# Kernel tuning notes

Hardware: AMD Instinct MI355X
Metric: run time of the kernel (lower is better)

The kernel has to match this reference:

```python
import jax, jax.numpy as jnp
import numpy as np

NS, B, T, S, H, V, G = 30, 16, 8, 400, 400, 20000, 3


def setup_inputs() -> dict:
    key = jax.random.key(0)
    ks = jax.random.split(key, 16)
    f = lambda k, shp, s: jax.random.normal(k, shp, jnp.float32) * s
    return dict(
        encoded_hidden=f(ks[0], (B, H), 1.0),
        encoded_outputs=f(ks[1], (B, S, H), 1.0),
        slot_emb=f(ks[2], (NS, H), 0.1),
        emb=f(ks[3], (V, H), 0.1),
        W_ih=f(ks[4], (3 * H, H), 0.05),
        W_hh=f(ks[5], (3 * H, H), 0.05),
        b_ih=jnp.zeros((3 * H,), jnp.float32),
        b_hh=jnp.zeros((3 * H,), jnp.float32),
        W_ratio_w=f(ks[6], (1, 3 * H), 0.05),
        W_ratio_b=jnp.zeros((1,), jnp.float32),
        W_gate_w=f(ks[7], (G, H), 0.05),
        W_gate_b=jnp.zeros((G,), jnp.float32),
        story=jax.random.randint(ks[8], (B, S), 0, V),
        target=jax.random.randint(ks[9], (B, NS, T), 0, V),
        encoded_lens=jax.random.randint(ks[10], (B,), S // 2, S + 1).astype(jnp.int32),
    )


def reference(encoded_hidden, encoded_outputs, slot_emb, emb, W_ih, W_hh, b_ih, b_hh,
              W_ratio_w, W_ratio_b, W_gate_w, W_gate_b, story, target, encoded_lens):
    ns, h = slot_emb.shape
    b, s, _ = encoded_outputs.shape
    t = target.shape[2]
    v = emb.shape[0]
    bs = ns * b  # fused slot*batch decode rows (parallel_decode)

    enc_out = jnp.tile(encoded_outputs, (ns, 1, 1))            # [bs,S,H]
    story_r = jnp.tile(story, (ns, 1))                          # [bs,S]
    lens_r = jnp.tile(encoded_lens, (ns,))                      # [bs]
    mask = jnp.arange(s)[None, :] < lens_r[:, None]             # [bs,S]
    h0 = jnp.tile(encoded_hidden, (ns, 1))                      # [bs,H]
    x0 = jnp.broadcast_to(slot_emb[:, None, :], (ns, b, h)).reshape(bs, h)
    # teacher-forcing inputs, slot-major flatten like target[:, :, wi].T.flatten()
    tf_in = emb[jnp.transpose(target, (2, 1, 0)).reshape(t, bs)]  # [T,bs,H]
    row = jnp.arange(bs)[:, None]
    neg_inf = jnp.float32(-jnp.inf)

    def gru_cell(x, hid):
        gi = x @ W_ih.T + b_ih
        gh = hid @ W_hh.T + b_hh
        ir, iz, inn = jnp.split(gi, 3, axis=-1)
        hr, hz, hn = jnp.split(gh, 3, axis=-1)
        r = jax.nn.sigmoid(ir + hr)
        z = jax.nn.sigmoid(iz + hz)
        n = jnp.tanh(inn + r * hn)
        return (1.0 - z) * n + z * hid

    def step(carry, x_next):
        hid, x = carry
        h_new = gru_cell(x, hid)                                # dec_state == hidden for 1-step GRU
        scores = jnp.einsum('bh,bsh->bs', h_new, enc_out)
        scores = jnp.where(mask, scores, neg_inf)
        prob = jax.nn.softmax(scores, axis=1)
        context = jnp.einsum('bs,bsh->bh', prob, enc_out)
        p_vocab = jax.nn.softmax(h_new @ emb.T, axis=1)         # [bs,V]
        p_gen_vec = jnp.concatenate([h_new, context, x], axis=-1)
        switch = jax.nn.sigmoid(p_gen_vec @ W_ratio_w.T + W_ratio_b)  # [bs,1]
        p_ctx = jnp.zeros((bs, v), p_vocab.dtype).at[row, story_r].add(prob)
        final = (1.0 - switch) * p_ctx + switch * p_vocab
        gate = context @ W_gate_w.T + W_gate_b
        return (h_new, x_next), (final, gate)

    _, (finals, gates) = jax.lax.scan(step, (h0, x0), tf_in)
    all_point = finals.reshape(t, ns, b, v).transpose(1, 2, 0, 3)  # [NS,B,T,V]
    all_gate = gates[0].reshape(ns, b, -1)                          # gates from wi==0
    return all_point, all_gate
```

## Files before the change

kernel.cpp:

```cpp
#include <hip/hip_runtime.h>
#include <hip/hip_bf16.h>

#define NSLOT 30
#define BB    16
#define TT    8
#define SS    400
#define HH    400
#define KP    416
#define NKK   13
#define VV    20000
#define GG    3
#define BSR   480
#define NBN   157
#define NCT   1256
#define NG2   1200
#define NCT2  75
#define NRT   30
#define FRAG_STRIDE 512

typedef unsigned short u16;
typedef __attribute__((ext_vector_type(8))) short bf16x8;
typedef __attribute__((ext_vector_type(4))) float f32x4;

__device__ __forceinline__ short f2bfs(float f){
  __hip_bfloat16 h = __float2bfloat16(f);
  union { __hip_bfloat16 b; short u; } v; v.b = h; return v.u;
}
__device__ __forceinline__ unsigned int pack2(float lo, float hi){
  return (unsigned int)(u16)f2bfs(lo) | ((unsigned int)(u16)f2bfs(hi) << 16);
}
__device__ __forceinline__ float bfu(u16 u){
  union { unsigned int i; float f; } v; v.i = ((unsigned int)u) << 16; return v.f;
}
__device__ __forceinline__ float bfu_lo(unsigned int u){
  union { unsigned int i; float f; } v; v.i = u << 16; return v.f;
}
__device__ __forceinline__ float bfu_hi(unsigned int u){
  union { unsigned int i; float f; } v; v.i = u & 0xffff0000u; return v.f;
}
__device__ __forceinline__ float sigm(float x){ return 1.f / (1.f + __expf(-x)); }
__device__ __forceinline__ float tanh_fast(float x){
  float e = __expf(2.f * x);
  return 1.f - 2.f / (e + 1.f);
}
__device__ __forceinline__ float wred_max(float v){
  #pragma unroll
  for (int off = 32; off; off >>= 1) v = fmaxf(v, __shfl_xor(v, off, 64));
  return v;
}
__device__ __forceinline__ float wred_sum(float v){
  #pragma unroll
  for (int off = 32; off; off >>= 1) v += __shfl_xor(v, off, 64);
  return v;
}

__global__ __launch_bounds__(256) void k_init(const float* __restrict__ eh,
                                              const float* __restrict__ semb,
                                              float* __restrict__ h_ws,
                                              float* __restrict__ x_ws)
{
  int idx = blockIdx.x * 256 + threadIdx.x;
  if (idx >= BSR * HH) return;
  int r = idx / HH, k = idx - r * HH;
  int batch = r % BB, slot = r / BB;
  h_ws[idx] = eh[batch * HH + k];
  x_ws[idx] = semb[slot * HH + k];
}

__global__ __launch_bounds__(256) void k_split_xh(
    const float* __restrict__ h_ws, const float* __restrict__ x_ws,
    short* __restrict__ h_hi, short* __restrict__ h_lo,
    short* __restrict__ x_hi, short* __restrict__ x_lo)
{
  const int NU = NRT * NKK * 64;
  for (int u = blockIdx.x * 256 + threadIdx.x; u < 2 * NU; u += gridDim.x * 256){
    int uu = u; int sel = 0;
    if (uu >= NU){ uu -= NU; sel = 1; }
    const float* S = sel ? x_ws : h_ws;
    short* ph = sel ? x_hi : h_hi;
    short* pl = sel ? x_lo : h_lo;
    int lane = uu & 63, kt = uu >> 6;
    int rtile = kt / NKK, kk = kt - rtile * NKK;
    int lg = lane >> 4, rl = lane & 15;
    int r = rtile * 16 + rl, k = kk * 32 + lg * 8;
    bf16x8 oh, ol;
    #pragma unroll
    for (int j = 0; j < 8; ++j){
      if (k + j < HH){
        float v = S[(size_t)r * HH + k + j];
        short hb = f2bfs(v);
        oh[j] = hb; ol[j] = f2bfs(v - bfu((u16)hb));
      } else { oh[j] = 0; ol[j] = 0; }
    }
    *reinterpret_cast<bf16x8*>(ph + (size_t)uu * 8) = oh;
    *reinterpret_cast<bf16x8*>(pl + (size_t)uu * 8) = ol;
  }
}

__global__ __launch_bounds__(256) void k_cast_W(
    const float* __restrict__ Wih, const float* __restrict__ Whh,
    short* __restrict__ Wih_hi, short* __restrict__ Wih_lo,
    short* __restrict__ Whh_hi, short* __restrict__ Whh_lo)
{
  const int NU = NCT2 * NKK * 64;
  for (int u = blockIdx.x * 256 + threadIdx.x; u < 2 * NU; u += gridDim.x * 256){
    int uu = u; int sel = 0;
    if (uu >= NU){ uu -= NU; sel = 1; }
    const float* W = sel ? Whh : Wih;
    short* ph = sel ? Whh_hi : Wih_hi;
    short* pl = sel ? Whh_lo : Wih_lo;
    int lane = uu & 63, kt = uu >> 6;
    int ctile = kt / NKK, kk = kt - ctile * NKK;
    int lg = lane >> 4, cl = lane & 15;
    int c = ctile * 16 + cl, k = kk * 32 + lg * 8;
    bf16x8 oh, ol;
    #pragma unroll
    for (int j = 0; j < 8; ++j){
      if (k + j < HH){
        float v = W[(size_t)c * HH + k + j];
        short hb = f2bfs(v);
        oh[j] = hb; ol[j] = f2bfs(v - bfu((u16)hb));
      } else { oh[j] = 0; ol[j] = 0; }
    }
    *reinterpret_cast<bf16x8*>(ph + (size_t)uu * 8) = oh;
    *reinterpret_cast<bf16x8*>(pl + (size_t)uu * 8) = ol;
  }
}

__global__ __launch_bounds__(256) void k_cast_emb(const float* __restrict__ emb,
                                                  short* __restrict__ ebf)
{
  const int nunit = NCT * NKK * 64;
  for (int u = blockIdx.x * 256 + threadIdx.x; u < nunit; u += gridDim.x * 256){
    int lane = u & 63;
    int kt = u >> 6;
    int ctile = kt / NKK, kk = kt - ctile * NKK;
    int lg = lane >> 4, cl = lane & 15;
    int c = ctile * 16 + cl;
    int k = kk * 32 + lg * 8;
    bf16x8 o;
    if (c < VV && k < HH){
      const float* src = emb + (size_t)c * HH + k;
      #pragma unroll
      for (int j = 0; j < 8; ++j) o[j] = f2bfs(src[j]);
    } else {
      #pragma unroll
      for (int j = 0; j < 8; ++j) o[j] = 0;
    }
    *reinterpret_cast<bf16x8*>(ebf + (size_t)u * 8) = o;
  }
}

__global__ __launch_bounds__(256) void k_gemm2_mfma(
    const short* __restrict__ x_hi, const short* __restrict__ x_lo,
    const short* __restrict__ h_hi, const short* __restrict__ h_lo,
    const short* __restrict__ Wih_hi, const short* __restrict__ Wih_lo,
    const short* __restrict__ Whh_hi, const short* __restrict__ Whh_lo,
    float* __restrict__ gi, float* __restrict__ gh)
{
  const int t = threadIdx.x;
  const int lane = t & 63, wid = t >> 6;
  const int wr = wid >> 1, wc = wid & 1;
  const int l15 = lane & 15, lg = lane >> 4;
  const int bM = blockIdx.x, bN = blockIdx.y, z = blockIdx.z;

  const short* A_hi = z ? h_hi : x_hi;
  const short* A_lo = z ? h_lo : x_lo;
  const short* B_hi = z ? Whh_hi : Wih_hi;
  const short* B_lo = z ? Whh_lo : Wih_lo;
  float* C = z ? gh : gi;

  const short *ah[4], *al[4], *bh[4], *bl[4];
  #pragma unroll
  for (int m = 0; m < 4; ++m){
    int rtile = min(bM * 8 + wr * 4 + m, NRT - 1);
    size_t off = (size_t)rtile * (NKK * FRAG_STRIDE) + lane * 8;
    ah[m] = A_hi + off; al[m] = A_lo + off;
  }
  #pragma unroll
  for (int n = 0; n < 4; ++n){
    int ctile = min(bN * 8 + wc * 4 + n, NCT2 - 1);
    size_t off = (size_t)ctile * (NKK * FRAG_STRIDE) + lane * 8;
    bh[n] = B_hi + off; bl[n] = B_lo + off;
  }

  f32x4 acc[4][4];
  #pragma unroll
  for (int m = 0; m < 4; ++m)
    #pragma unroll
    for (int n = 0; n < 4; ++n)
      acc[m][n] = (f32x4){0.f, 0.f, 0.f, 0.f};

  #pragma unroll
  for (int kk = 0; kk < NKK; ++kk){
    const int ko = kk * FRAG_STRIDE;
    bf16x8 ah_r[4], al_r[4];
    #pragma unroll
    for (int m = 0; m < 4; ++m){
      ah_r[m] = *reinterpret_cast<const bf16x8*>(ah[m] + ko);
      al_r[m] = *reinterpret_cast<const bf16x8*>(al[m] + ko);
    }
    #pragma unroll
    for (int n = 0; n < 4; ++n){
      bf16x8 bhv = *reinterpret_cast<const bf16x8*>(bh[n] + ko);
      bf16x8 blv = *reinterpret_cast<const bf16x8*>(bl[n] + ko);
      #pragma unroll
      for (int m = 0; m < 4; ++m){
        acc[m][n] = __builtin_amdgcn_mfma_f32_16x16x32_bf16(ah_r[m], bhv, acc[m][n], 0, 0, 0);
        acc[m][n] = __builtin_amdgcn_mfma_f32_16x16x32_bf16(ah_r[m], blv, acc[m][n], 0, 0, 0);
        acc[m][n] = __builtin_amdgcn_mfma_f32_16x16x32_bf16(al_r[m], bhv, acc[m][n], 0, 0, 0);
      }
    }
  }

  #pragma unroll
  for (int m = 0; m < 4; ++m){
    #pragma unroll
    for (int q = 0; q < 4; ++q){
      int row = bM * 128 + wr * 64 + m * 16 + lg * 4 + q;
      if (row < BSR){
        #pragma unroll
        for (int n = 0; n < 4; ++n){
          int col = bN * 128 + wc * 64 + n * 16 + l15;
          if (col < NG2) C[(size_t)row * NG2 + col] = acc[m][n][q];
        }
      }
    }
  }
}

__global__ __launch_bounds__(256) void k_logits_mfma(
    const short* __restrict__ hbf, const short* __restrict__ ebf,
    float* __restrict__ out, float* __restrict__ pmax_ws,
    float* __restrict__ psum_ws, int wi)
{
  const int t = threadIdx.x;
  const int lane = t & 63, wid = t >> 6;
  const int wr = wid >> 1, wc = wid & 1;
  const int l15 = lane & 15, lg = lane >> 4;
  const int bM = blockIdx.x, bN = blockIdx.y;

  const short* ap[4];
  const short* bp[4];
  #pragma unroll
  for (int m = 0; m < 4; ++m){
    int rtile = bM * 8 + wr * 4 + m;
    ap[m] = hbf + (size_t)min(rtile, NRT - 1) * (NKK * FRAG_STRIDE) + lane * 8;
  }
  #pragma unroll
  for (int n = 0; n < 4; ++n){
    int ctile = bN * 8 + wc * 4 + n;
    bp[n] = ebf + (size_t)ctile * (NKK * FRAG_STRIDE) + lane * 8;
  }

  f32x4 acc[4][4];
  #pragma unroll
  for (int m = 0; m < 4; ++m)
    #pragma unroll
    for (int n = 0; n < 4; ++n)
      acc[m][n] = (f32x4){0.f, 0.f, 0.f, 0.f};

  #pragma unroll
  for (int kk = 0; kk < NKK; ++kk){
    const int ko = kk * FRAG_STRIDE;
    bf16x8 a[4];
    #pragma unroll
    for (int m = 0; m < 4; ++m)
      a[m] = *reinterpret_cast<const bf16x8*>(ap[m] + ko);
    #pragma unroll
    for (int n = 0; n < 4; ++n){
      bf16x8 b = *reinterpret_cast<const bf16x8*>(bp[n] + ko);
      #pragma unroll
      for (int m = 0; m < 4; ++m)
        acc[m][n] = __builtin_amdgcn_mfma_f32_16x16x32_bf16(a[m], b, acc[m][n], 0, 0, 0);
    }
  }

  #pragma unroll
  for (int m = 0; m < 4; ++m){
    #pragma unroll
    for (int q = 0; q < 4; ++q){
      int row = bM * 128 + wr * 64 + m * 16 + lg * 4 + q;
      u16* lrow16 = reinterpret_cast<u16*>(out + ((size_t)row * TT + wi) * VV);
      #pragma unroll
      for (int n = 0; n < 4; ++n){
        float v = acc[m][n][q];
        float vp = __shfl_xor(v, 1, 64);
        int col = bN * 128 + wc * 64 + n * 16 + l15;
        if (((l15 & 1) == 0) && row < BSR && col < VV)
          *reinterpret_cast<unsigned int*>(lrow16 + col) = pack2(v, vp);
      }
    }
    f32x4 rmax, rsum;
    #pragma unroll
    for (int q = 0; q < 4; ++q){
      float mx = -3.0e38f;
      #pragma unroll
      for (int n = 0; n < 4; ++n){
        int col = bN * 128 + wc * 64 + n * 16 + l15;
        float v = (col < VV) ? acc[m][n][q] : -3.0e38f;
        mx = fmaxf(mx, v);
      }
      #pragma unroll
      for (int off = 1; off < 16; off <<= 1) mx = fmaxf(mx, __shfl_xor(mx, off, 64));
      float sm = 0.f;
      #pragma unroll
      for (int n = 0; n < 4; ++n){
        int col = bN * 128 + wc * 64 + n * 16 + l15;
        if (col < VV) sm += __expf(acc[m][n][q] - mx);
      }
      #pragma unroll
      for (int off = 1; off < 16; off <<= 1) sm += __shfl_xor(sm, off, 64);
      rmax[q] = mx; rsum[q] = sm;
    }
    if (l15 == 0){
      #pragma unroll
      for (int q = 0; q < 4; ++q){
        int row = bM * 128 + wr * 64 + m * 16 + lg * 4 + q;
        if (row < BSR){
          size_t pidx = ((size_t)row * NBN + bN) * 2 + wc;
          pmax_ws[pidx] = rmax[q];
          psum_ws[pidx] = rsum[q];
        }
      }
    }
  }
}

__global__ __launch_bounds__(256) void k_att(
    const float* __restrict__ enc, const float* __restrict__ emb,
    const float* __restrict__ b_ih, const float* __restrict__ b_hh,
    const float* __restrict__ Wr_w, const float* __restrict__ Wr_b,
    const float* __restrict__ Wg_w, const float* __restrict__ Wg_b,
    const int* __restrict__ target, const int* __restrict__ lens,
    const float* __restrict__ gi_ws, const float* __restrict__ gh_ws,
    float* __restrict__ h_ws, float* __restrict__ x_ws,
    short* __restrict__ h_hi, short* __restrict__ h_lo,
    short* __restrict__ x_hi, short* __restrict__ x_lo,
    float* __restrict__ prob_ws, float* __restrict__ sw_ws,
    float* __restrict__ d_out, int wi)
{
  __shared__ float hn_s[HH];
  __shared__ float sc_s[SS];
  __shared__ float ctx_s[HH];
  __shared__ float red[4];
  __shared__ float redg[GG][4];

  const int t = threadIdx.x;
  const int rg = blockIdx.x;
  const int batch = rg % BB, slot = rg / BB;
  const int len = lens[batch];
  const int rtile = rg >> 4, rl = rg & 15;

  const float* gir = gi_ws + (size_t)rg * NG2;
  const float* ghr = gh_ws + (size_t)rg * NG2;
  for (int k = t; k < HH; k += 256){
    float irv = gir[k]          + b_ih[k];
    float izv = gir[HH + k]     + b_ih[HH + k];
    float inv = gir[2 * HH + k] + b_ih[2 * HH + k];
    float hrv = ghr[k]          + b_hh[k];
    float hzv = ghr[HH + k]     + b_hh[HH + k];
    float hnv = ghr[2 * HH + k] + b_hh[2 * HH + k];
    float rr = sigm(irv + hrv);
    float zz = sigm(izv + hzv);
    float nn = tanh_fast(inv + rr * hnv);
    float hold = h_ws[(size_t)rg * HH + k];
    float hnew = (1.f - zz) * nn + zz * hold;
    hn_s[k] = hnew;
    h_ws[(size_t)rg * HH + k] = hnew;
  }
  __syncthreads();

  if (t < KP / 8){
    const int kk = t >> 2, lg = t & 3;
    bf16x8 oh, ol;
    #pragma unroll
    for (int j = 0; j < 8; ++j){
      int k = t * 8 + j;
      if (k < HH){
        float v = hn_s[k];
        short hb = f2bfs(v);
        oh[j] = hb; ol[j] = f2bfs(v - bfu((u16)hb));
      } else { oh[j] = 0; ol[j] = 0; }
    }
    size_t off = ((size_t)rtile * NKK + kk) * FRAG_STRIDE + (lg * 16 + rl) * 8;
    *reinterpret_cast<bf16x8*>(h_hi + off) = oh;
    *reinterpret_cast<bf16x8*>(h_lo + off) = ol;
  }

  const float* encb = enc + (size_t)batch * SS * HH;
  float lmax = -3.0e38f;
  for (int s = t; s < SS; s += 256){
    if (s < len){
      const float4* er4 = reinterpret_cast<const float4*>(encb + (size_t)s * HH);
      float dot = 0.f;
      for (int k4 = 0; k4 < HH / 4; ++k4){
        float4 e = er4[k4];
        float4 hv = *reinterpret_cast<const float4*>(&hn_s[k4 * 4]);
        dot += e.x*hv.x + e.y*hv.y + e.z*hv.z + e.w*hv.w;
      }
      sc_s[s] = dot;
      lmax = fmaxf(lmax, dot);
    }
  }
  lmax = wred_max(lmax);
  if ((t & 63) == 0) red[t >> 6] = lmax;
  __syncthreads();
  lmax = fmaxf(fmaxf(red[0], red[1]), fmaxf(red[2], red[3]));
  float lsum = 0.f;
  for (int s = t; s < SS; s += 256){
    float e = (s < len) ? __expf(sc_s[s] - lmax) : 0.f;
    sc_s[s] = e;
    lsum += e;
  }
  lsum = wred_sum(lsum);
  __syncthreads();
  if ((t & 63) == 0) red[t >> 6] = lsum;
  __syncthreads();
  lsum = red[0] + red[1] + red[2] + red[3];
  float invl = 1.f / lsum;
  for (int s = t; s < SS; s += 256){
    float p = sc_s[s] * invl;
    sc_s[s] = p;
    prob_ws[(size_t)rg * SS + s] = p;
  }
  __syncthreads();

  for (int k = t; k < HH; k += 256){
    float c0 = 0.f, c1 = 0.f, c2 = 0.f, c3 = 0.f;
    const float* ek = encb + k;
    int s = 0;
    for (; s + 3 < len; s += 4){
      c0 += sc_s[s]     * ek[(size_t)s * HH];
      c1 += sc_s[s + 1] * ek[(size_t)(s + 1) * HH];
      c2 += sc_s[s + 2] * ek[(size_t)(s + 2) * HH];
      c3 += sc_s[s + 3] * ek[(size_t)(s + 3) * HH];
    }
    for (; s < len; ++s) c0 += sc_s[s] * ek[(size_t)s * HH];
    ctx_s[k] = (c0 + c1) + (c2 + c3);
  }
  __syncthreads();

  float sa = 0.f;
  for (int k = t; k < HH; k += 256){
    sa += Wr_w[k]          * hn_s[k]
        + Wr_w[HH + k]     * ctx_s[k]
        + Wr_w[2 * HH + k] * x_ws[(size_t)rg * HH + k];
  }
  sa = wred_sum(sa);
  if ((t & 63) == 0) red[t >> 6] = sa;
  __syncthreads();
  sa = red[0] + red[1] + red[2] + red[3];
  if (t == 0) sw_ws[rg] = sigm(sa + Wr_b[0]);

  if (wi == 0){
    float ga[GG] = {0.f, 0.f, 0.f};
    for (int k = t; k < HH; k += 256){
      float cv = ctx_s[k];
      ga[0] += Wg_w[k] * cv;
      ga[1] += Wg_w[HH + k] * cv;
      ga[2] += Wg_w[2 * HH + k] * cv;
    }
    #pragma unroll
    for (int g = 0; g < GG; ++g){
      ga[g] = wred_sum(ga[g]);
      if ((t & 63) == 0) redg[g][t >> 6] = ga[g];
    }
    __syncthreads();
    if (t < GG)
      d_out[(size_t)NSLOT * BB * TT * VV + (size_t)rg * GG + t] =
          redg[t][0] + redg[t][1] + redg[t][2] + redg[t][3] + Wg_b[t];
  }

  const int tgt = target[batch * (NSLOT * TT) + slot * TT + wi];
  const float* embrow = emb + (size_t)tgt * HH;
  for (int k = t; k < HH; k += 256)
    x_ws[(size_t)rg * HH + k] = embrow[k];
  if (t < KP / 8){
    const int kk = t >> 2, lg = t & 3;
    bf16x8 oh, ol;
    #pragma unroll
    for (int j = 0; j < 8; ++j){
      int k = t * 8 + j;
      if (k < HH){
        float v = embrow[k];
        short hb = f2bfs(v);
        oh[j] = hb; ol[j] = f2bfs(v - bfu((u16)hb));
      } else { oh[j] = 0; ol[j] = 0; }
    }
    size_t off = ((size_t)rtile * NKK + kk) * FRAG_STRIDE + (lg * 16 + rl) * 8;
    *reinterpret_cast<bf16x8*>(x_hi + off) = oh;
    *reinterpret_cast<bf16x8*>(x_lo + off) = ol;
  }
}

__global__ __launch_bounds__(256) void k_finalize(
    float* __restrict__ logits_out, const float* __restrict__ prob_ws,
    const float* __restrict__ pmax_ws, const float* __restrict__ psum_ws,
    const float* __restrict__ sw_ws, const int* __restrict__ story,
    const int* __restrict__ lens, int wi)
{
  __shared__ float pctx[VV];
  __shared__ float red[4];
  const int t = threadIdx.x;
  const int r = blockIdx.x;
  const int batch = r % BB;
  for (int v = t; v < VV; v += 256) pctx[v] = 0.f;
  __syncthreads();
  const int len = lens[batch];
  for (int s = t; s < SS; s += 256){
    if (s < len)
      atomicAdd(&pctx[story[batch * SS + s]], prob_ws[(size_t)r * SS + s]);
  }

  float* lrow = logits_out + ((size_t)r * TT + wi) * VV;
  const uint4* l16 = reinterpret_cast<const uint4*>(lrow);
  uint4 stage[10];
  {
    int ns = 0;
    for (int i = t; i < VV / 8; i += 256) stage[ns++] = l16[i];
  }

  const float* pm = pmax_ws + (size_t)r * (NBN * 2);
  const float* ps = psum_ws + (size_t)r * (NBN * 2);
  float m = -3.0e38f;
  for (int i = t; i < NBN * 2; i += 256) m = fmaxf(m, pm[i]);
  m = wred_max(m);
  if ((t & 63) == 0) red[t >> 6] = m;
  __syncthreads();
  m = fmaxf(fmaxf(red[0], red[1]), fmaxf(red[2], red[3]));
  float lsum = 0.f;
  for (int i = t; i < NBN * 2; i += 256) lsum += ps[i] * __expf(pm[i] - m);
  lsum = wred_sum(lsum);
  __syncthreads();
  if ((t & 63) == 0) red[t >> 6] = lsum;
  __syncthreads();
  lsum = red[0] + red[1] + red[2] + red[3];

  const float sw = sw_ws[r];
  const float invl = sw / lsum;
  const float osw = 1.f - sw;
  {
    int ns = 0;
    for (int i = t; i < VV / 8; i += 256){
      uint4 q = stage[ns++];
      int v = i * 8;
      float4 o0, o1;
      o0.x = __expf(bfu_lo(q.x) - m) * invl + osw * pctx[v + 0];
      o0.y = __expf(bfu_hi(q.x) - m) * invl + osw * pctx[v + 1];
      o0.z = __expf(bfu_lo(q.y) - m) * invl + osw * pctx[v + 2];
      o0.w = __expf(bfu_hi(q.y) - m) * invl + osw * pctx[v + 3];
      o1.x = __expf(bfu_lo(q.z) - m) * invl + osw * pctx[v + 4];
      o1.y = __expf(bfu_hi(q.z) - m) * invl + osw * pctx[v + 5];
      o1.z = __expf(bfu_lo(q.w) - m) * invl + osw * pctx[v + 6];
      o1.w = __expf(bfu_hi(q.w) - m) * invl + osw * pctx[v + 7];
      *reinterpret_cast<float4*>(lrow + v)     = o0;
      *reinterpret_cast<float4*>(lrow + v + 4) = o1;
    }
  }
}

extern "C" void kernel_launch(void* const* d_in, const int* in_sizes, int n_in,
                              void* d_out, int out_size, void* d_ws, size_t ws_size,
                              hipStream_t stream)
{
  (void)in_sizes; (void)n_in; (void)out_size; (void)ws_size;
  const float* eh    = (const float*)d_in[0];
  const float* enc   = (const float*)d_in[1];
  const float* semb  = (const float*)d_in[2];
  const float* emb   = (const float*)d_in[3];
  const float* W_ih  = (const float*)d_in[4];
  const float* W_hh  = (const float*)d_in[5];
  const float* b_ih  = (const float*)d_in[6];
  const float* b_hh  = (const float*)d_in[7];
  const float* Wr_w  = (const float*)d_in[8];
  const float* Wr_b  = (const float*)d_in[9];
  const float* Wg_w  = (const float*)d_in[10];
  const float* Wg_b  = (const float*)d_in[11];
  const int* story = (const int*)d_in[12];
  const int* tgt   = (const int*)d_in[13];
  const int* lens  = (const int*)d_in[14];
  float* out = (float*)d_out;

  float* ws      = (float*)d_ws;
  float* h_ws    = ws;
  float* x_ws    = ws + 192000;
  float* prob_ws = ws + 384000;
  float* sw_ws   = ws + 576000;
  float* gi_ws   = ws + 576512;
  float* gh_ws   = ws + 1152512;
  float* pmax_ws = ws + 1728512;
  float* psum_ws = ws + 1879552;
  short* h_hi    = (short*)(ws + 2030592);
  short* emb_bf  = (short*)(ws + 2130432);
  short* Wih_hi  = (short*)(ws + 6310400);
  short* Wih_lo  = (short*)(ws + 6560000);
  short* Whh_hi  = (short*)(ws + 6809600);
  short* Whh_lo  = (short*)(ws + 7059200);
  short* x_hi    = (short*)(ws + 7308800);
  short* x_lo    = (short*)(ws + 7408640);
  short* h_lo    = (short*)(ws + 7508480);

  k_cast_emb<<<2048, 256, 0, stream>>>(emb, emb_bf);
  k_cast_W<<<512, 256, 0, stream>>>(W_ih, W_hh, Wih_hi, Wih_lo, Whh_hi, Whh_lo);
  k_init<<<750, 256, 0, stream>>>(eh, semb, h_ws, x_ws);
  k_split_xh<<<195, 256, 0, stream>>>(h_ws, x_ws, h_hi, h_lo, x_hi, x_lo);
  for (int wi = 0; wi < TT; ++wi){
    dim3 gg(4, 10, 2);
    k_gemm2_mfma<<<gg, 256, 0, stream>>>(x_hi, x_lo, h_hi, h_lo,
                                         Wih_hi, Wih_lo, Whh_hi, Whh_lo,
                                         gi_ws, gh_ws);
    k_att<<<BSR, 256, 0, stream>>>(enc, emb, b_ih, b_hh, Wr_w, Wr_b, Wg_w, Wg_b,
                                   tgt, lens, gi_ws, gh_ws, h_ws, x_ws,
                                   h_hi, h_lo, x_hi, x_lo,
                                   prob_ws, sw_ws, out, wi);
    dim3 gl(4, NBN);
    k_logits_mfma<<<gl, 256, 0, stream>>>(h_hi, emb_bf, out, pmax_ws, psum_ws, wi);
    k_finalize<<<BSR, 256, 0, stream>>>(out, prob_ws, pmax_ws, psum_ws,
                                        sw_ws, story, lens, wi);
  }
}
```

Baseline: 997.7 us.

## Fuse next-step GRU GEMM into finalize kernel and merge init kernels

```diff
diff --git a/kernel.cpp b/kernel.cpp
--- a/kernel.cpp
+++ b/kernel.cpp
@@ -54,21 +54,9 @@
   return v;
 }
 
-__global__ __launch_bounds__(256) void k_init(const float* __restrict__ eh,
-                                              const float* __restrict__ semb,
-                                              float* __restrict__ h_ws,
-                                              float* __restrict__ x_ws)
-{
-  int idx = blockIdx.x * 256 + threadIdx.x;
-  if (idx >= BSR * HH) return;
-  int r = idx / HH, k = idx - r * HH;
-  int batch = r % BB, slot = r / BB;
-  h_ws[idx] = eh[batch * HH + k];
-  x_ws[idx] = semb[slot * HH + k];
-}
-
-__global__ __launch_bounds__(256) void k_split_xh(
-    const float* __restrict__ h_ws, const float* __restrict__ x_ws,
+__global__ __launch_bounds__(256) void k_init_all(
+    const float* __restrict__ eh, const float* __restrict__ semb,
+    float* __restrict__ h_ws, float* __restrict__ x_ws,
     short* __restrict__ h_hi, short* __restrict__ h_lo,
     short* __restrict__ x_hi, short* __restrict__ x_lo)
 {
@@ -76,20 +64,23 @@
   for (int u = blockIdx.x * 256 + threadIdx.x; u < 2 * NU; u += gridDim.x * 256){
     int uu = u; int sel = 0;
     if (uu >= NU){ uu -= NU; sel = 1; }
-    const float* S = sel ? x_ws : h_ws;
     short* ph = sel ? x_hi : h_hi;
     short* pl = sel ? x_lo : h_lo;
+    float* fw = sel ? x_ws : h_ws;
     int lane = uu & 63, kt = uu >> 6;
     int rtile = kt / NKK, kk = kt - rtile * NKK;
     int lg = lane >> 4, rl = lane & 15;
     int r = rtile * 16 + rl, k = kk * 32 + lg * 8;
+    const float* src = sel ? (semb + (size_t)rtile * HH)
+                           : (eh   + (size_t)rl * HH);
     bf16x8 oh, ol;
     #pragma unroll
     for (int j = 0; j < 8; ++j){
       if (k + j < HH){
-        float v = S[(size_t)r * HH + k + j];
+        float v = src[k + j];
         short hb = f2bfs(v);
         oh[j] = hb; ol[j] = f2bfs(v - bfu((u16)hb));
+        fw[(size_t)r * HH + k + j] = v;
       } else { oh[j] = 0; ol[j] = 0; }
     }
     *reinterpret_cast<bf16x8*>(ph + (size_t)uu * 8) = oh;
@@ -151,18 +142,17 @@
   }
 }
 
-__global__ __launch_bounds__(256) void k_gemm2_mfma(
+__device__ __forceinline__ void gemm2_body(
+    int bM, int bN, int z, int t,
     const short* __restrict__ x_hi, const short* __restrict__ x_lo,
     const short* __restrict__ h_hi, const short* __restrict__ h_lo,
     const short* __restrict__ Wih_hi, const short* __restrict__ Wih_lo,
     const short* __restrict__ Whh_hi, const short* __restrict__ Whh_lo,
     float* __restrict__ gi, float* __restrict__ gh)
 {
-  const int t = threadIdx.x;
   const int lane = t & 63, wid = t >> 6;
   const int wr = wid >> 1, wc = wid & 1;
   const int l15 = lane & 15, lg = lane >> 4;
-  const int bM = blockIdx.x, bN = blockIdx.y, z = blockIdx.z;
 
   const short* A_hi = z ? h_hi : x_hi;
   const short* A_lo = z ? h_lo : x_lo;
@@ -227,6 +217,17 @@
       }
     }
   }
+}
+
+__global__ __launch_bounds__(256) void k_gemm2_mfma(
+    const short* __restrict__ x_hi, const short* __restrict__ x_lo,
+    const short* __restrict__ h_hi, const short* __restrict__ h_lo,
+    const short* __restrict__ Wih_hi, const short* __restrict__ Wih_lo,
+    const short* __restrict__ Whh_hi, const short* __restrict__ Whh_lo,
+    float* __restrict__ gi, float* __restrict__ gh)
+{
+  gemm2_body(blockIdx.x, blockIdx.y, blockIdx.z, threadIdx.x,
+             x_hi, x_lo, h_hi, h_lo, Wih_hi, Wih_lo, Whh_hi, Whh_lo, gi, gh);
 }
 
 __global__ __launch_bounds__(256) void k_logits_mfma(
@@ -494,15 +495,30 @@
   }
 }
 
-__global__ __launch_bounds__(256) void k_finalize(
+__global__ __launch_bounds__(256) void k_fin_gemm2(
     float* __restrict__ logits_out, const float* __restrict__ prob_ws,
     const float* __restrict__ pmax_ws, const float* __restrict__ psum_ws,
     const float* __restrict__ sw_ws, const int* __restrict__ story,
-    const int* __restrict__ lens, int wi)
+    const int* __restrict__ lens, int wi,
+    const short* __restrict__ x_hi, const short* __restrict__ x_lo,
+    const short* __restrict__ h_hi, const short* __restrict__ h_lo,
+    const short* __restrict__ Wih_hi, const short* __restrict__ Wih_lo,
+    const short* __restrict__ Whh_hi, const short* __restrict__ Whh_lo,
+    float* __restrict__ gi, float* __restrict__ gh, int do_gemm)
 {
   __shared__ float pctx[VV];
   __shared__ float red[4];
   const int t = threadIdx.x;
+
+  if (blockIdx.x >= BSR){
+    if (!do_gemm) return;
+    int b = blockIdx.x - BSR;
+    int bM = b & 3, bN = (b >> 2) % 10, z = b / 40;
+    gemm2_body(bM, bN, z, t, x_hi, x_lo, h_hi, h_lo,
+               Wih_hi, Wih_lo, Whh_hi, Whh_lo, gi, gh);
+    return;
+  }
+
   const int r = blockIdx.x;
   const int batch = r % BB;
   for (int v = t; v < VV; v += 256) pctx[v] = 0.f;
@@ -603,20 +619,23 @@
 
   k_cast_emb<<<2048, 256, 0, stream>>>(emb, emb_bf);
   k_cast_W<<<512, 256, 0, stream>>>(W_ih, W_hh, Wih_hi, Wih_lo, Whh_hi, Whh_lo);
-  k_init<<<750, 256, 0, stream>>>(eh, semb, h_ws, x_ws);
-  k_split_xh<<<195, 256, 0, stream>>>(h_ws, x_ws, h_hi, h_lo, x_hi, x_lo);
+  k_init_all<<<195, 256, 0, stream>>>(eh, semb, h_ws, x_ws,
+                                      h_hi, h_lo, x_hi, x_lo);
+  dim3 gg(4, 10, 2);
+  k_gemm2_mfma<<<gg, 256, 0, stream>>>(x_hi, x_lo, h_hi, h_lo,
+                                       Wih_hi, Wih_lo, Whh_hi, Whh_lo,
+                                       gi_ws, gh_ws);
   for (int wi = 0; wi < TT; ++wi){
-    dim3 gg(4, 10, 2);
-    k_gemm2_mfma<<<gg, 256, 0, stream>>>(x_hi, x_lo, h_hi, h_lo,
-                                         Wih_hi, Wih_lo, Whh_hi, Whh_lo,
-                                         gi_ws, gh_ws);
     k_att<<<BSR, 256, 0, stream>>>(enc, emb, b_ih, b_hh, Wr_w, Wr_b, Wg_w, Wg_b,
                                    tgt, lens, gi_ws, gh_ws, h_ws, x_ws,
                                    h_hi, h_lo, x_hi, x_lo,
                                    prob_ws, sw_ws, out, wi);
     dim3 gl(4, NBN);
     k_logits_mfma<<<gl, 256, 0, stream>>>(h_hi, emb_bf, out, pmax_ws, psum_ws, wi);
-    k_finalize<<<BSR, 256, 0, stream>>>(out, prob_ws, pmax_ws, psum_ws,
-                                        sw_ws, story, lens, wi);
-  }
-}
+    k_fin_gemm2<<<BSR + 80, 256, 0, stream>>>(out, prob_ws, pmax_ws, psum_ws,
+                                              sw_ws, story, lens, wi,
+                                              x_hi, x_lo, h_hi, h_lo,
+                                              Wih_hi, Wih_lo, Whh_hi, Whh_lo,
+                                              gi_ws, gh_ws, (wi + 1 < TT) ? 1 : 0);
+  }
+}
```

Result: faster. 974.9 us (median of 3 runs) (-2.3%).
